# Optimization experiments

Hardware: AMD Instinct MI355X
Metric: run time of the kernel (lower is better)

The kernel has to match this reference:

```python
import jax, jax.numpy as jnp
import numpy as np

N_STEPS = 4   # wavelet steps
N_LIFT = 2    # lifting steps per wavelet step
B, N = 512, 65536
TAPS = 3


def setup_inputs() -> dict:
    key = jax.random.key(0)
    k1, k2, k3 = jax.random.split(key, 3)
    x = jax.random.normal(k1, (B, N), dtype=jnp.float32)
    # torch inits these to zeros; use small random values to exercise the math
    P_coeffs = jax.random.normal(k2, (N_STEPS * N_LIFT, TAPS), dtype=jnp.float32) * 0.1
    U_coeffs = jax.random.normal(k3, (N_STEPS * N_LIFT, TAPS), dtype=jnp.float32) * 0.1
    return {"x": x, "P_coeffs": P_coeffs, "U_coeffs": U_coeffs}


def _cconv(x, h):
    # circular convolution: y[n] = sum_k h[k] * x[(n-k) mod N]; h has 3 taps
    return sum(h[k] * jnp.roll(x, k, axis=-1) for k in range(TAPS))


def reference(x, P_coeffs, U_coeffs):
    zs = []
    lowpass = x
    for j in range(N_STEPS):
        # LazyWavelet: even/odd polyphase split
        evens = lowpass[:, 0::2]
        odds = lowpass[:, 1::2]
        # Lifting steps
        for k in range(N_LIFT):
            i = j * N_LIFT + k
            detail = odds - _cconv(evens, P_coeffs[i])
            average = evens + _cconv(detail, U_coeffs[i])
            evens, odds = average, detail
        # Wavelet.forward keeps coeffs[:,0] (average) as z, recurses on coeffs[:,1] (detail)
        zs.append(evens)
        lowpass = odds
    zs.append(lowpass)
    return tuple(zs)
```

## Files before the change

kernel.cpp:

```cpp
#include <hip/hip_runtime.h>

#define BS    256
#define CHUNK 4096
#define HALO  256
#define NN    65536
#define LDSF  6528

template<int M, int T, bool SYNC>
__device__ __forceinline__ void level_lift(float* lds, int inOff, int npairs,
                                           int avgOff, int detOff,
                                           const float* __restrict__ P6,
                                           const float* __restrict__ U6, int tid) {
  constexpr int W = M + 8;
  const bool act = (T == BS) || (tid < T);
  const int p0 = M * tid - 8;
  float in[2 * W];
  if (act) {
#pragma unroll
    for (int i = 0; i < W; ++i) {
      int p = p0 + i;
      p = p < 0 ? 0 : (p >= npairs ? npairs - 1 : p);
      float2 v = *(const float2*)&lds[inOff + 2 * p];
      in[2 * i] = v.x;
      in[2 * i + 1] = v.y;
    }
  }
  const float P0 = P6[0], P1 = P6[1], P2 = P6[2], P3 = P6[3], P4 = P6[4], P5 = P6[5];
  const float U0 = U6[0], U1 = U6[1], U2 = U6[2], U3 = U6[3], U4 = U6[4], U5 = U6[5];
  if (SYNC) __syncthreads();
  if (act) {
    float e1 = 0, e2 = 0, d1 = 0, d2 = 0, a1 = 0, a2 = 0, f1 = 0, f2 = 0;
#pragma unroll
    for (int i = 0; i < W; ++i) {
      float e0 = in[2 * i], o0 = in[2 * i + 1];
      float d0 = o0 - (P0 * e0 + P1 * e1 + P2 * e2);
      float a0 = e0 + (U0 * d0 + U1 * d1 + U2 * d2);
      float f0 = d0 - (P3 * a0 + P4 * a1 + P5 * a2);
      float b0 = a0 + (U3 * f0 + U4 * f1 + U5 * f2);
      if (i >= 8) {
        int p = p0 + i;
        if (p < npairs) {
          lds[avgOff + p] = b0;
          lds[detOff + p] = f0;
        }
      }
      e2 = e1; e1 = e0; d2 = d1; d1 = d0; a2 = a1; a1 = a0; f2 = f1; f1 = f0;
    }
  }
}

__device__ __forceinline__ void store4r(float* dst, const float* src, int n4,
                                        int tid, int t0) {
  if (tid >= t0) {
    const float4* s = (const float4*)src;
    float4* d = (float4*)dst;
    for (int i = tid - t0; i < n4; i += (BS - t0)) d[i] = s[i];
  }
}

__global__ __launch_bounds__(BS)
void wavelet_fused_kernel(const float* __restrict__ x,
                          const float* __restrict__ Pc,
                          const float* __restrict__ Uc,
                          float* __restrict__ out) {
  __shared__ __align__(16) float A[LDSF];

  const int tid  = threadIdx.x;
  const int wave = tid >> 6;
  const int lane = tid & 63;
  const int cx   = blockIdx.x;
  const int row  = blockIdx.y;
  const int S    = cx * CHUNK;

  {
    const float4* x4 = (const float4*)(x + (size_t)row * NN);
    const int base4 = ((S - HALO) & (NN - 1)) >> 2;
    for (int s = wave; s < 17; s += 4) {
      const float4* g = &x4[(base4 + s * 64 + lane) & (NN / 4 - 1)];
      float* l = &A[s * 256];
      __builtin_amdgcn_global_load_lds(
          (const __attribute__((address_space(1))) void*)g,
          (__attribute__((address_space(3))) void*)l, 16, 0, 0);
    }
  }
  __syncthreads();

  float* z0 = out + (size_t)row * 32768 + (S >> 1);
  float* z1 = out + 16777216 + (size_t)row * 16384 + (S >> 2);
  float* z2 = out + 25165824 + (size_t)row * 8192 + (S >> 3);
  float* z3 = out + 29360128 + (size_t)row * 4096 + (S >> 4);
  float* z4 = out + 31457280 + (size_t)row * 4096 + (S >> 4);

  level_lift<9, 256, true>(A, 0, 2176, 0, 2176, Pc, Uc, tid);
  __syncthreads();

  store4r(z0, A + 128, 512, tid, 128);
  level_lift<9, 128, false>(A, 2176, 1088, 4352, 5440, Pc + 6, Uc + 6, tid);
  __syncthreads();

  store4r(z1, A + 4416, 256, tid, 64);
  level_lift<9, 64, false>(A, 5440, 544, 0, 544, Pc + 12, Uc + 12, tid);
  __syncthreads();

  store4r(z2, A + 32, 128, tid, 64);
  level_lift<5, 64, false>(A, 544, 272, 1088, 1360, Pc + 18, Uc + 18, tid);
  __syncthreads();

  store4r(z3, A + 1104, 64, tid, 0);
  store4r(z4, A + 1376, 64, tid, 0);
}

extern "C" void kernel_launch(void* const* d_in, const int* in_sizes, int n_in,
                              void* d_out, int out_size, void* d_ws, size_t ws_size,
                              hipStream_t stream) {
  const float* x  = (const float*)d_in[0];
  const float* Pc = (const float*)d_in[1];
  const float* Uc = (const float*)d_in[2];
  float* out = (float*)d_out;

  dim3 grid(NN / CHUNK, 512, 1);
  dim3 block(BS, 1, 1);
  wavelet_fused_kernel<<<grid, block, 0, stream>>>(x, Pc, Uc, out);
}
```

Measured before the change: 48.73 us.

## Give each wave its own independent chunk to eliminate block-wide barriers

Restructures the fused wavelet kernel so each 64-lane wave processes its own 1024-sample chunk with a private LDS slice and its own halo. Block-wide __syncthreads are replaced by wave-local lgkmcnt/vmcnt waits. All lanes stay active at every level instead of idling as the level shrinks. The cost is a larger halo overhead (256 halo per 1024 samples instead of per 4096), so more redundant global loads and compute.

```diff
diff --git a/kernel.cpp b/kernel.cpp
--- a/kernel.cpp
+++ b/kernel.cpp
@@ -1,61 +1,54 @@
 #include <hip/hip_runtime.h>
 
 #define BS    256
-#define CHUNK 4096
+#define WC    1024
 #define HALO  256
 #define NN    65536
-#define LDSF  6528
+#define WFL   1280
 
-template<int M, int T, bool SYNC>
-__device__ __forceinline__ void level_lift(float* lds, int inOff, int npairs,
-                                           int avgOff, int detOff,
-                                           const float* __restrict__ P6,
-                                           const float* __restrict__ U6, int tid) {
+#define WAVE_FENCE() do { \
+    asm volatile("s_waitcnt lgkmcnt(0)" ::: "memory"); \
+    __builtin_amdgcn_sched_barrier(0); \
+  } while (0)
+
+template<int M, int NPAIRS>
+__device__ __forceinline__ void wave_lift(float* wA, int inOff, int avgOff,
+                                          int detOff,
+                                          const float* __restrict__ P6,
+                                          const float* __restrict__ U6,
+                                          int lane) {
   constexpr int W = M + 8;
-  const bool act = (T == BS) || (tid < T);
-  const int p0 = M * tid - 8;
   float in[2 * W];
-  if (act) {
+  const int p0 = M * lane - 8;
 #pragma unroll
-    for (int i = 0; i < W; ++i) {
-      int p = p0 + i;
-      p = p < 0 ? 0 : (p >= npairs ? npairs - 1 : p);
-      float2 v = *(const float2*)&lds[inOff + 2 * p];
-      in[2 * i] = v.x;
-      in[2 * i + 1] = v.y;
-    }
+  for (int i = 0; i < W; ++i) {
+    int p = p0 + i;
+    p = p < 0 ? 0 : (p >= NPAIRS ? NPAIRS - 1 : p);
+    float2 v = *(const float2*)&wA[inOff + 2 * p];
+    in[2 * i] = v.x;
+    in[2 * i + 1] = v.y;
   }
   const float P0 = P6[0], P1 = P6[1], P2 = P6[2], P3 = P6[3], P4 = P6[4], P5 = P6[5];
   const float U0 = U6[0], U1 = U6[1], U2 = U6[2], U3 = U6[3], U4 = U6[4], U5 = U6[5];
-  if (SYNC) __syncthreads();
-  if (act) {
-    float e1 = 0, e2 = 0, d1 = 0, d2 = 0, a1 = 0, a2 = 0, f1 = 0, f2 = 0;
+  WAVE_FENCE();
+  float e1 = 0, e2 = 0, d1 = 0, d2 = 0, a1 = 0, a2 = 0, f1 = 0, f2 = 0;
 #pragma unroll
-    for (int i = 0; i < W; ++i) {
-      float e0 = in[2 * i], o0 = in[2 * i + 1];
-      float d0 = o0 - (P0 * e0 + P1 * e1 + P2 * e2);
-      float a0 = e0 + (U0 * d0 + U1 * d1 + U2 * d2);
-      float f0 = d0 - (P3 * a0 + P4 * a1 + P5 * a2);
-      float b0 = a0 + (U3 * f0 + U4 * f1 + U5 * f2);
-      if (i >= 8) {
-        int p = p0 + i;
-        if (p < npairs) {
-          lds[avgOff + p] = b0;
-          lds[detOff + p] = f0;
-        }
+  for (int i = 0; i < W; ++i) {
+    float e0 = in[2 * i], o0 = in[2 * i + 1];
+    float d0 = o0 - (P0 * e0 + P1 * e1 + P2 * e2);
+    float a0 = e0 + (U0 * d0 + U1 * d1 + U2 * d2);
+    float f0 = d0 - (P3 * a0 + P4 * a1 + P5 * a2);
+    float b0 = a0 + (U3 * f0 + U4 * f1 + U5 * f2);
+    if (i >= 8) {
+      int p = p0 + i;
+      if (p < NPAIRS) {
+        wA[avgOff + p] = b0;
+        wA[detOff + p] = f0;
       }
-      e2 = e1; e1 = e0; d2 = d1; d1 = d0; a2 = a1; a1 = a0; f2 = f1; f1 = f0;
     }
+    e2 = e1; e1 = e0; d2 = d1; d1 = d0; a2 = a1; a1 = a0; f2 = f1; f1 = f0;
   }
-}
-
-__device__ __forceinline__ void store4r(float* dst, const float* src, int n4,
-                                        int tid, int t0) {
-  if (tid >= t0) {
-    const float4* s = (const float4*)src;
-    float4* d = (float4*)dst;
-    for (int i = tid - t0; i < n4; i += (BS - t0)) d[i] = s[i];
-  }
+  WAVE_FENCE();
 }
 
 __global__ __launch_bounds__(BS)
@@ -63,51 +56,53 @@
                           const float* __restrict__ Pc,
                           const float* __restrict__ Uc,
                           float* __restrict__ out) {
-  __shared__ __align__(16) float A[LDSF];
+  __shared__ __align__(16) float A[4 * WFL];
 
   const int tid  = threadIdx.x;
   const int wave = tid >> 6;
   const int lane = tid & 63;
-  const int cx   = blockIdx.x;
+  const int gc   = blockIdx.x * 4 + wave;
   const int row  = blockIdx.y;
-  const int S    = cx * CHUNK;
+  float* wA = A + wave * WFL;
 
+  const float4* x4 = (const float4*)(x + (size_t)row * NN);
+  const int base4 = ((gc * WC - HALO) & (NN - 1)) >> 2;
+#pragma unroll
+  for (int s = 0; s < 5; ++s) {
+    const float4* g = &x4[(base4 + s * 64 + lane) & (NN / 4 - 1)];
+    __builtin_amdgcn_global_load_lds(
+        (const __attribute__((address_space(1))) void*)g,
+        (__attribute__((address_space(3))) void*)&wA[s * 256], 16, 0, 0);
+  }
+  asm volatile("s_waitcnt vmcnt(0)" ::: "memory");
+  __builtin_amdgcn_sched_barrier(0);
+
+  wave_lift<10, 640>(wA, 0, 0, 640, Pc, Uc, lane);
   {
-    const float4* x4 = (const float4*)(x + (size_t)row * NN);
-    const int base4 = ((S - HALO) & (NN - 1)) >> 2;
-    for (int s = wave; s < 17; s += 4) {
-      const float4* g = &x4[(base4 + s * 64 + lane) & (NN / 4 - 1)];
-      float* l = &A[s * 256];
-      __builtin_amdgcn_global_load_lds(
-          (const __attribute__((address_space(1))) void*)g,
-          (__attribute__((address_space(3))) void*)l, 16, 0, 0);
-    }
+    float4* d = (float4*)(out + (size_t)row * 32768 + gc * 512);
+    d[lane]      = *(const float4*)&wA[128 + 4 * lane];
+    d[lane + 64] = *(const float4*)&wA[384 + 4 * lane];
   }
-  __syncthreads();
 
-  float* z0 = out + (size_t)row * 32768 + (S >> 1);
-  float* z1 = out + 16777216 + (size_t)row * 16384 + (S >> 2);
-  float* z2 = out + 25165824 + (size_t)row * 8192 + (S >> 3);
-  float* z3 = out + 29360128 + (size_t)row * 4096 + (S >> 4);
-  float* z4 = out + 31457280 + (size_t)row * 4096 + (S >> 4);
+  wave_lift<5, 320>(wA, 640, 640, 960, Pc + 6, Uc + 6, lane);
+  {
+    float4* d = (float4*)(out + 16777216 + (size_t)row * 16384 + gc * 256);
+    d[lane] = *(const float4*)&wA[704 + 4 * lane];
+  }
 
-  level_lift<9, 256, true>(A, 0, 2176, 0, 2176, Pc, Uc, tid);
-  __syncthreads();
+  wave_lift<3, 160>(wA, 960, 960, 1120, Pc + 12, Uc + 12, lane);
+  {
+    float2* d = (float2*)(out + 25165824 + (size_t)row * 8192 + gc * 128);
+    d[lane] = *(const float2*)&wA[992 + 2 * lane];
+  }
 
-  store4r(z0, A + 128, 512, tid, 128);
-  level_lift<9, 128, false>(A, 2176, 1088, 4352, 5440, Pc + 6, Uc + 6, tid);
-  __syncthreads();
-
-  store4r(z1, A + 4416, 256, tid, 64);
-  level_lift<9, 64, false>(A, 5440, 544, 0, 544, Pc + 12, Uc + 12, tid);
-  __syncthreads();
-
-  store4r(z2, A + 32, 128, tid, 64);
-  level_lift<5, 64, false>(A, 544, 272, 1088, 1360, Pc + 18, Uc + 18, tid);
-  __syncthreads();
-
-  store4r(z3, A + 1104, 64, tid, 0);
-  store4r(z4, A + 1376, 64, tid, 0);
+  wave_lift<2, 80>(wA, 1120, 1120, 1200, Pc + 18, Uc + 18, lane);
+  {
+    float* d3 = out + 29360128 + (size_t)row * 4096 + gc * 64;
+    float* d4 = out + 31457280 + (size_t)row * 4096 + gc * 64;
+    d3[lane] = wA[1136 + lane];
+    d4[lane] = wA[1216 + lane];
+  }
 }
 
 extern "C" void kernel_launch(void* const* d_in, const int* in_sizes, int n_in,
@@ -118,7 +113,7 @@
   const float* Uc = (const float*)d_in[2];
   float* out = (float*)d_out;
 
-  dim3 grid(NN / CHUNK, 512, 1);
+  dim3 grid(NN / WC / 4, 512, 1);
   dim3 block(BS, 1, 1);
   wavelet_fused_kernel<<<grid, block, 0, stream>>>(x, Pc, Uc, out);
 }
```

Measured after the change: 56.18 us. +15.3%, slower.

## Halve chunk and block size, compact LDS layout, split read/write phases

Applied to the files above, without the earlier changes.

Shrinks each block to 128 threads processing a 2048-sample chunk with a 256-sample halo, cutting LDS use from about 25 KB to 9 KB and requesting 8 blocks per SM through launch bounds, so more blocks can be resident. The lifting helper is split into separate read and write phases. In each later level, one wave computes the next level while the other wave stores the previous level's output to global memory. The cost is a larger halo fraction: the same 256-sample halo now serves half as many samples, so more input is loaded and recomputed per output, and twice as many blocks are launched.

```diff
diff --git a/kernel.cpp b/kernel.cpp
--- a/kernel.cpp
+++ b/kernel.cpp
@@ -1,64 +1,51 @@
 #include <hip/hip_runtime.h>
 
-#define BS    256
-#define CHUNK 4096
+#define BS    128
+#define CHUNK 2048
 #define HALO  256
 #define NN    65536
-#define LDSF  6528
+#define LDSF  2304
 
-template<int M, int T, bool SYNC>
-__device__ __forceinline__ void level_lift(float* lds, int inOff, int npairs,
-                                           int avgOff, int detOff,
-                                           const float* __restrict__ P6,
-                                           const float* __restrict__ U6, int tid) {
-  constexpr int W = M + 8;
-  const bool act = (T == BS) || (tid < T);
-  const int p0 = M * tid - 8;
-  float in[2 * W];
-  if (act) {
+template<int M, int NP>
+__device__ __forceinline__ void lift_read(const float* __restrict__ A, int inOff,
+                                          int t, float* __restrict__ in) {
+  const int p0 = M * t - 8;
 #pragma unroll
-    for (int i = 0; i < W; ++i) {
-      int p = p0 + i;
-      p = p < 0 ? 0 : (p >= npairs ? npairs - 1 : p);
-      float2 v = *(const float2*)&lds[inOff + 2 * p];
-      in[2 * i] = v.x;
-      in[2 * i + 1] = v.y;
-    }
-  }
-  const float P0 = P6[0], P1 = P6[1], P2 = P6[2], P3 = P6[3], P4 = P6[4], P5 = P6[5];
-  const float U0 = U6[0], U1 = U6[1], U2 = U6[2], U3 = U6[3], U4 = U6[4], U5 = U6[5];
-  if (SYNC) __syncthreads();
-  if (act) {
-    float e1 = 0, e2 = 0, d1 = 0, d2 = 0, a1 = 0, a2 = 0, f1 = 0, f2 = 0;
-#pragma unroll
-    for (int i = 0; i < W; ++i) {
-      float e0 = in[2 * i], o0 = in[2 * i + 1];
-      float d0 = o0 - (P0 * e0 + P1 * e1 + P2 * e2);
-      float a0 = e0 + (U0 * d0 + U1 * d1 + U2 * d2);
-      float f0 = d0 - (P3 * a0 + P4 * a1 + P5 * a2);
-      float b0 = a0 + (U3 * f0 + U4 * f1 + U5 * f2);
-      if (i >= 8) {
-        int p = p0 + i;
-        if (p < npairs) {
-          lds[avgOff + p] = b0;
-          lds[detOff + p] = f0;
-        }
-      }
-      e2 = e1; e1 = e0; d2 = d1; d1 = d0; a2 = a1; a1 = a0; f2 = f1; f1 = f0;
-    }
+  for (int i = 0; i < M + 8; ++i) {
+    int p = p0 + i;
+    p = p < 0 ? 0 : (p >= NP ? NP - 1 : p);
+    float2 v = *(const float2*)&A[inOff + 2 * p];
+    in[2 * i] = v.x;
+    in[2 * i + 1] = v.y;
   }
 }
 
-__device__ __forceinline__ void store4r(float* dst, const float* src, int n4,
-                                        int tid, int t0) {
-  if (tid >= t0) {
-    const float4* s = (const float4*)src;
-    float4* d = (float4*)dst;
-    for (int i = tid - t0; i < n4; i += (BS - t0)) d[i] = s[i];
+template<int M, int NP>
+__device__ __forceinline__ void lift_write(float* __restrict__ A, int avgOff,
+                                           int detOff, int t,
+                                           const float* __restrict__ in,
+                                           const float* __restrict__ P6,
+                                           const float* __restrict__ U6) {
+  const float P0 = P6[0], P1 = P6[1], P2 = P6[2], P3 = P6[3], P4 = P6[4], P5 = P6[5];
+  const float U0 = U6[0], U1 = U6[1], U2 = U6[2], U3 = U6[3], U4 = U6[4], U5 = U6[5];
+  const int p0 = M * t - 8;
+  float e1 = 0, e2 = 0, d1 = 0, d2 = 0, a1 = 0, a2 = 0, f1 = 0, f2 = 0;
+#pragma unroll
+  for (int i = 0; i < M + 8; ++i) {
+    float e0 = in[2 * i], o0 = in[2 * i + 1];
+    float d0 = o0 - (P0 * e0 + P1 * e1 + P2 * e2);
+    float a0 = e0 + (U0 * d0 + U1 * d1 + U2 * d2);
+    float f0 = d0 - (P3 * a0 + P4 * a1 + P5 * a2);
+    float b0 = a0 + (U3 * f0 + U4 * f1 + U5 * f2);
+    if (i >= 8) {
+      int p = p0 + i;
+      if (p < NP) { A[avgOff + p] = b0; A[detOff + p] = f0; }
+    }
+    e2 = e1; e1 = e0; d2 = d1; d1 = d0; a2 = a1; a1 = a0; f2 = f1; f1 = f0;
   }
 }
 
-__global__ __launch_bounds__(BS)
+__global__ __launch_bounds__(BS, 8)
 void wavelet_fused_kernel(const float* __restrict__ x,
                           const float* __restrict__ Pc,
                           const float* __restrict__ Uc,
@@ -75,39 +62,66 @@
   {
     const float4* x4 = (const float4*)(x + (size_t)row * NN);
     const int base4 = ((S - HALO) & (NN - 1)) >> 2;
-    for (int s = wave; s < 17; s += 4) {
+    for (int s = wave; s < 9; s += 2) {
       const float4* g = &x4[(base4 + s * 64 + lane) & (NN / 4 - 1)];
-      float* l = &A[s * 256];
       __builtin_amdgcn_global_load_lds(
           (const __attribute__((address_space(1))) void*)g,
-          (__attribute__((address_space(3))) void*)l, 16, 0, 0);
+          (__attribute__((address_space(3))) void*)&A[s * 256], 16, 0, 0);
     }
   }
   __syncthreads();
 
-  float* z0 = out + (size_t)row * 32768 + (S >> 1);
-  float* z1 = out + 16777216 + (size_t)row * 16384 + (S >> 2);
-  float* z2 = out + 25165824 + (size_t)row * 8192 + (S >> 3);
-  float* z3 = out + 29360128 + (size_t)row * 4096 + (S >> 4);
-  float* z4 = out + 31457280 + (size_t)row * 4096 + (S >> 4);
+  float4* z0 = (float4*)out + (size_t)row * 8192 + (S >> 3);
+  float4* z1 = (float4*)out + 4194304 + row * 4096 + (S >> 4);
+  float4* z2 = (float4*)out + 6291456 + row * 2048 + (S >> 5);
+  float4* z3 = (float4*)out + 7340032 + row * 1024 + (S >> 6);
+  float4* z4 = (float4*)out + 7864320 + row * 1024 + (S >> 6);
 
-  level_lift<9, 256, true>(A, 0, 2176, 0, 2176, Pc, Uc, tid);
+  {
+    float in0[34];
+    lift_read<9, 1152>(A, 0, tid, in0);
+    __syncthreads();
+    lift_write<9, 1152>(A, 0, 1152, tid, in0, Pc, Uc);
+  }
   __syncthreads();
 
-  store4r(z0, A + 128, 512, tid, 128);
-  level_lift<9, 128, false>(A, 2176, 1088, 4352, 5440, Pc + 6, Uc + 6, tid);
+  float in1[34];
+  if (tid < 64) {
+    lift_read<9, 576>(A, 1152, tid, in1);
+  } else {
+    const int t = tid - 64;
+#pragma unroll
+    for (int k = 0; k < 4; ++k) z0[t + 64 * k] = *(const float4*)&A[128 + 4 * (t + 64 * k)];
+  }
+  __syncthreads();
+  if (tid < 64) lift_write<9, 576>(A, 1152, 1728, tid, in1, Pc + 6, Uc + 6);
   __syncthreads();
 
-  store4r(z1, A + 4416, 256, tid, 64);
-  level_lift<9, 64, false>(A, 5440, 544, 0, 544, Pc + 12, Uc + 12, tid);
+  float in2[26];
+  if (tid < 64) {
+    lift_read<5, 288>(A, 1728, tid, in2);
+  } else {
+    const int t = tid - 64;
+#pragma unroll
+    for (int k = 0; k < 2; ++k) z1[t + 64 * k] = *(const float4*)&A[1216 + 4 * (t + 64 * k)];
+  }
+  __syncthreads();
+  if (tid < 64) lift_write<5, 288>(A, 1728, 2016, tid, in2, Pc + 12, Uc + 12);
   __syncthreads();
 
-  store4r(z2, A + 32, 128, tid, 64);
-  level_lift<5, 64, false>(A, 544, 272, 1088, 1360, Pc + 18, Uc + 18, tid);
+  float in3[22];
+  if (tid < 64) {
+    lift_read<3, 144>(A, 2016, tid, in3);
+  } else {
+    const int t = tid - 64;
+    z2[t] = *(const float4*)&A[1760 + 4 * t];
+  }
+  __syncthreads();
+  if (tid < 64) lift_write<3, 144>(A, 2016, 2160, tid, in3, Pc + 18, Uc + 18);
   __syncthreads();
 
-  store4r(z3, A + 1104, 64, tid, 0);
-  store4r(z4, A + 1376, 64, tid, 0);
+  if (tid < 32)                     z3[tid]      = *(const float4*)&A[2032 + 4 * tid];
+  else if (tid >= 64 && tid < 96)   z4[tid - 64] = *(const float4*)&A[2176 + 4 * (tid - 64)];
 }
 
 extern "C" void kernel_launch(void* const* d_in, const int* in_sizes, int n_in,
```

New measurement: 49.74 us. 1.02x slower.
